# Kernel tuning notes

Hardware: AMD Instinct MI355X
Metric: run time of the kernel (lower is better)

Reference implementation:

```python
import jax, jax.numpy as jnp
import numpy as np

N_NODES = 100000
N_COMM = 1024
N_EDGES = 3200000
D_IN = 128
D_OUT = 128


def setup_inputs() -> dict:
    key = jax.random.key(0)
    k1, k2, k3, k4, k5, k6 = jax.random.split(key, 6)
    x = jax.random.normal(k1, (N_NODES + N_COMM, D_IN), dtype=jnp.float32)
    weight = jax.random.normal(k2, (D_IN, D_OUT), dtype=jnp.float32) * (1.0 / np.sqrt(D_IN))
    # assignments must be positive so row/col sums are nonzero
    assignments = jax.random.uniform(k3, (N_NODES, N_COMM), dtype=jnp.float32)
    edge_row = jax.random.randint(k4, (N_EDGES,), 0, N_NODES, dtype=jnp.int32)
    edge_col = jax.random.randint(k5, (N_EDGES,), 0, N_NODES, dtype=jnp.int32)
    edge_val = jax.random.uniform(k6, (N_EDGES,), dtype=jnp.float32)
    return {"x": x, "weight": weight, "assignments": assignments,
            "edge_row": edge_row, "edge_col": edge_col, "edge_val": edge_val}


def reference(x, weight, assignments, edge_row, edge_col, edge_val):
    N, C = assignments.shape
    support = x @ weight                      # [N+C, D_OUT]
    sup_nodes = support[:N]                   # node rows (support[:-C])
    sup_comm = support[N:]                    # community rows (support[-C:])

    # row-normalized assignments @ community support
    a_norm = assignments / assignments.sum(axis=1, keepdims=True)  # [N, C]
    comm_to_node = a_norm @ sup_comm                               # [N, D_OUT]

    # sparse adj @ node support via COO gather + segment scatter-add
    msgs = edge_val[:, None] * sup_nodes[edge_col]                 # [E, D_OUT]
    spmm = jax.ops.segment_sum(msgs, edge_row, num_segments=N)     # [N, D_OUT]

    output1 = comm_to_node + spmm                                  # [N, D_OUT]

    # row-normalized assignments.T @ node support
    at = assignments.T                                             # [C, N]
    at_norm = at / at.sum(axis=1, keepdims=True)
    output2 = at_norm @ sup_nodes                                  # [C, D_OUT]

    return jnp.concatenate((output1, output2), axis=0)            # [N+C, D_OUT]
```

## Files before the change

kernel.cpp:

```cpp
#include <hip/hip_runtime.h>
#include <hip/hip_fp16.h>

#define NN 100000
#define NC 1024
#define NM 101024
#define NE 3200000
#define DD 128

typedef __attribute__((ext_vector_type(8))) short s16x8;
typedef __attribute__((ext_vector_type(4))) float f32x4;

#define MFMA __builtin_amdgcn_mfma_f32_16x16x32_bf16

__device__ __forceinline__ short f2bf(float f) {
  unsigned u = __float_as_uint(f);
  u = (u + 0x7FFFu + ((u >> 16) & 1u)) >> 16;
  return (short)u;
}
__device__ __forceinline__ float bf2f(short h) {
  return __uint_as_float(((unsigned)(unsigned short)h) << 16);
}

__global__ __launch_bounds__(256) void k_zero(int* __restrict__ p, int n) {
  int t = blockIdx.x * 256 + threadIdx.x;
  if (t < n) p[t] = 0;
}

__global__ __launch_bounds__(256) void k_wpack(const float* __restrict__ W,
                                               short* __restrict__ wh,
                                               short* __restrict__ wl) {
  int t = blockIdx.x * 256 + threadIdx.x;
  int k = t >> 7, d = t & 127;
  float v = W[t];
  short h = f2bf(v);
  short l = f2bf(v - bf2f(h));
  int idx = (((k >> 5) * 8 + (d >> 4)) * 64 + ((k >> 3) & 3) * 16 + (d & 15)) * 8 + (k & 7);
  wh[idx] = h;
  wl[idx] = l;
}

__global__ __launch_bounds__(256) void k_support(const float* __restrict__ x,
                                                 const short* __restrict__ wh,
                                                 const short* __restrict__ wl,
                                                 float* __restrict__ sup) {
  int wave = threadIdx.x >> 6, lane = threadIdx.x & 63;
  int r0 = blockIdx.x * 64 + wave * 16;
  int arow = r0 + (lane & 15);
  if (arow >= NM) arow = NM - 1;
  int kb = (lane >> 4) * 8;
  f32x4 acc[8];
  #pragma unroll
  for (int dt = 0; dt < 8; ++dt)
    #pragma unroll
    for (int q = 0; q < 4; ++q) acc[dt][q] = 0.f;

  #pragma unroll
  for (int ks = 0; ks < 4; ++ks) {
    const float* ap = x + (size_t)arow * DD + ks * 32 + kb;
    float4 v0 = *(const float4*)ap;
    float4 v1 = *(const float4*)(ap + 4);
    float vv[8] = {v0.x, v0.y, v0.z, v0.w, v1.x, v1.y, v1.z, v1.w};
    s16x8 xh, xl;
    #pragma unroll
    for (int j = 0; j < 8; ++j) {
      short h = f2bf(vv[j]);
      xh[j] = h;
      xl[j] = f2bf(vv[j] - bf2f(h));
    }
    const short* bph = wh + ks * 4096 + lane * 8;
    const short* bpl = wl + ks * 4096 + lane * 8;
    #pragma unroll
    for (int dt = 0; dt < 8; ++dt) {
      s16x8 bh = *(const s16x8*)(bph + dt * 512);
      s16x8 bl = *(const s16x8*)(bpl + dt * 512);
      acc[dt] = MFMA(xh, bh, acc[dt], 0, 0, 0);
      acc[dt] = MFMA(xl, bh, acc[dt], 0, 0, 0);
      acc[dt] = MFMA(xh, bl, acc[dt], 0, 0, 0);
    }
  }
  int rg = (lane >> 4) * 4, cc = lane & 15;
  #pragma unroll
  for (int dt = 0; dt < 8; ++dt)
    #pragma unroll
    for (int q = 0; q < 4; ++q) {
      int rr = r0 + rg + q;
      if (rr < NM) sup[(size_t)rr * DD + dt * 16 + cc] = acc[dt][q];
    }
}

__global__ __launch_bounds__(256) void k_suph(const float* __restrict__ sup,
                                              unsigned* __restrict__ suph) {
  int t = blockIdx.x * 256 + threadIdx.x;
  float2 f = *(const float2*)(sup + (size_t)t * 2);
  __half2 h = __floats2half2_rn(f.x, f.y);
  suph[t] = *(unsigned*)&h;
}

__global__ __launch_bounds__(256) void k_spack(const float* __restrict__ sup,
                                               short* __restrict__ bpk) {
  int t = blockIdx.x * 256 + threadIdx.x;
  int d = t & 127, ib = t >> 7;
  int rb = ib >> 2, g = ib & 3;
  s16x8 o;
  #pragma unroll
  for (int j = 0; j < 8; ++j) o[j] = f2bf(sup[(size_t)(ib * 8 + j) * DD + d]);
  *(s16x8*)(bpk + (size_t)((rb * 8 + (d >> 4)) * 64 + g * 16 + (d & 15)) * 8) = o;
}

__global__ __launch_bounds__(256) void k_u1(const float* __restrict__ A,
                                            const short* __restrict__ bpk,
                                            float* __restrict__ out) {
  __shared__ float rsh[128];
  int wave = threadIdx.x >> 6, lane = threadIdx.x & 63;
  int r0 = blockIdx.x * 128 + wave * 32;
  int kb = (lane >> 4) * 8;
  f32x4 acc[2][8];
  #pragma unroll
  for (int m = 0; m < 2; ++m)
    #pragma unroll
    for (int dt = 0; dt < 8; ++dt)
      #pragma unroll
      for (int q = 0; q < 4; ++q) acc[m][dt][q] = 0.f;
  float rs[2] = {0.f, 0.f};
  int row[2];
  #pragma unroll
  for (int m = 0; m < 2; ++m) {
    int r = r0 + m * 16 + (lane & 15);
    row[m] = (r < NN) ? r : NN - 1;
  }
  for (int ks = 0; ks < 32; ++ks) {
    s16x8 af[2];
    #pragma unroll
    for (int m = 0; m < 2; ++m) {
      const float* ap = A + (size_t)row[m] * NC + ks * 32 + kb;
      float4 v0 = *(const float4*)ap;
      float4 v1 = *(const float4*)(ap + 4);
      rs[m] += v0.x + v0.y + v0.z + v0.w + v1.x + v1.y + v1.z + v1.w;
      af[m][0] = f2bf(v0.x); af[m][1] = f2bf(v0.y);
      af[m][2] = f2bf(v0.z); af[m][3] = f2bf(v0.w);
      af[m][4] = f2bf(v1.x); af[m][5] = f2bf(v1.y);
      af[m][6] = f2bf(v1.z); af[m][7] = f2bf(v1.w);
    }
    const short* bp = bpk + (size_t)(3125 + ks) * 4096 + lane * 8;
    #pragma unroll
    for (int dt = 0; dt < 8; ++dt) {
      s16x8 b = *(const s16x8*)(bp + dt * 512);
      acc[0][dt] = MFMA(af[0], b, acc[0][dt], 0, 0, 0);
      acc[1][dt] = MFMA(af[1], b, acc[1][dt], 0, 0, 0);
    }
  }
  #pragma unroll
  for (int m = 0; m < 2; ++m) {
    float v = rs[m];
    v += __shfl_xor(v, 16);
    v += __shfl_xor(v, 32);
    if (lane < 16) rsh[wave * 32 + m * 16 + lane] = v;
  }
  __syncthreads();
  int rg = (lane >> 4) * 4, cc = lane & 15;
  #pragma unroll
  for (int m = 0; m < 2; ++m)
    #pragma unroll
    for (int q = 0; q < 4; ++q) {
      int wr = wave * 32 + m * 16 + rg + q;
      int r = blockIdx.x * 128 + wr;
      if (r < NN) {
        float inv = 1.f / rsh[wr];
        #pragma unroll
        for (int dt = 0; dt < 8; ++dt)
          out[(size_t)r * DD + dt * 16 + cc] = acc[m][dt][q] * inv;
      }
    }
}

__global__ __launch_bounds__(256) void k_u2(const float* __restrict__ A,
                                            const short* __restrict__ bpk,
                                            float* __restrict__ u2,
                                            float* __restrict__ csum) {
  __shared__ short atile[2][128 * 40];
  int wave = threadIdx.x >> 6, lane = threadIdx.x & 63;
  int c0 = (blockIdx.x & 7) * 128;
  int s = blockIdx.x >> 3;
  int wc = wave * 32;
  f32x4 acc[2][8];
  #pragma unroll
  for (int m = 0; m < 2; ++m)
    #pragma unroll
    for (int dt = 0; dt < 8; ++dt)
      #pragma unroll
      for (int q = 0; q < 4; ++q) acc[m][dt][q] = 0.f;
  float cs[2] = {0.f, 0.f};
  int ld_i = threadIdx.x >> 5;
  int ld_c = (threadIdx.x & 31) * 4;

  float4 rv[4];
  #pragma unroll
  for (int it = 0; it < 4; ++it)
    rv[it] = *(const float4*)(A + (size_t)(s * 800 + it * 8 + ld_i) * NC + c0 + ld_c);
  #pragma unroll
  for (int it = 0; it < 4; ++it) {
    int i = it * 8 + ld_i;
    atile[0][(ld_c + 0) * 40 + i] = f2bf(rv[it].x);
    atile[0][(ld_c + 1) * 40 + i] = f2bf(rv[it].y);
    atile[0][(ld_c + 2) * 40 + i] = f2bf(rv[it].z);
    atile[0][(ld_c + 3) * 40 + i] = f2bf(rv[it].w);
  }
  __syncthreads();

  for (int kk = 0; kk < 25; ++kk) {
    int p = kk & 1;
    if (kk < 24) {
      int i0n = s * 800 + (kk + 1) * 32;
      #pragma unroll
      for (int it = 0; it < 4; ++it)
        rv[it] = *(const float4*)(A + (size_t)(i0n + it * 8 + ld_i) * NC + c0 + ld_c);
    }
    s16x8 af[2];
    #pragma unroll
    for (int m = 0; m < 2; ++m) {
      af[m] = *(const s16x8*)(&atile[p][(wc + m * 16 + (lane & 15)) * 40 + (lane >> 4) * 8]);
      #pragma unroll
      for (int j = 0; j < 8; ++j) cs[m] += bf2f(af[m][j]);
    }
    if (kk < 24) {
      #pragma unroll
      for (int it = 0; it < 4; ++it) {
        int i = it * 8 + ld_i;
        atile[p ^ 1][(ld_c + 0) * 40 + i] = f2bf(rv[it].x);
        atile[p ^ 1][(ld_c + 1) * 40 + i] = f2bf(rv[it].y);
        atile[p ^ 1][(ld_c + 2) * 40 + i] = f2bf(rv[it].z);
        atile[p ^ 1][(ld_c + 3) * 40 + i] = f2bf(rv[it].w);
      }
    }
    const short* bp = bpk + (size_t)(s * 25 + kk) * 4096 + lane * 8;
    #pragma unroll
    for (int dt = 0; dt < 8; ++dt) {
      s16x8 b = *(const s16x8*)(bp + dt * 512);
      acc[0][dt] = MFMA(af[0], b, acc[0][dt], 0, 0, 0);
      acc[1][dt] = MFMA(af[1], b, acc[1][dt], 0, 0, 0);
    }
    __syncthreads();
  }
  #pragma unroll
  for (int m = 0; m < 2; ++m) {
    float v = cs[m];
    v += __shfl_xor(v, 16);
    v += __shfl_xor(v, 32);
    if (lane < 16) atomicAdd(&csum[c0 + wc + m * 16 + lane], v);
  }
  int rg = (lane >> 4) * 4, cc = lane & 15;
  #pragma unroll
  for (int m = 0; m < 2; ++m)
    #pragma unroll
    for (int dt = 0; dt < 8; ++dt)
      #pragma unroll
      for (int q = 0; q < 4; ++q)
        atomicAdd(&u2[(size_t)(c0 + wc + m * 16 + rg + q) * DD + dt * 16 + cc],
                  acc[m][dt][q]);
}

__global__ __launch_bounds__(256) void k_out2(const float* __restrict__ u2,
                                              const float* __restrict__ csum,
                                              float* __restrict__ out) {
  int t = blockIdx.x * 256 + threadIdx.x;
  int c = t >> 7;
  out[(size_t)(NN + c) * DD + (t & 127)] = u2[t] / csum[c];
}

__global__ __launch_bounds__(256) void k_hist(const int* __restrict__ er, int* __restrict__ hist) {
  int t = blockIdx.x * 256 + threadIdx.x;
  if (t < NE) atomicAdd(&hist[er[t]], 1);
}

__global__ __launch_bounds__(256) void k_scan1(const int* __restrict__ hist,
                                               int* __restrict__ excl,
                                               int* __restrict__ bsum) {
  __shared__ int sm[256];
  int t = threadIdx.x, g = blockIdx.x * 256 + t;
  int v = (g < NN) ? hist[g] : 0;
  sm[t] = v;
  __syncthreads();
  for (int off = 1; off < 256; off <<= 1) {
    int u = (t >= off) ? sm[t - off] : 0;
    __syncthreads();
    sm[t] += u;
    __syncthreads();
  }
  if (g < NN) excl[g] = sm[t] - v;
  if (t == 255) bsum[blockIdx.x] = sm[255];
}

__global__ __launch_bounds__(512) void k_scan2(const int* __restrict__ bsum,
                                               int* __restrict__ boff, int nb) {
  __shared__ int sm[512];
  int t = threadIdx.x;
  int v = (t < nb) ? bsum[t] : 0;
  sm[t] = v;
  __syncthreads();
  for (int off = 1; off < 512; off <<= 1) {
    int u = (t >= off) ? sm[t - off] : 0;
    __syncthreads();
    sm[t] += u;
    __syncthreads();
  }
  if (t < nb) boff[t] = sm[t] - v;
}

__global__ __launch_bounds__(256) void k_scan3(const int* __restrict__ excl,
                                               const int* __restrict__ boff,
                                               int* __restrict__ offs,
                                               int* __restrict__ cur) {
  int t = threadIdx.x, g = blockIdx.x * 256 + t;
  if (g < NN) {
    int o = excl[g] + boff[blockIdx.x];
    offs[g] = o;
    cur[g] = o;
  }
  if (g == 0) offs[NN] = NE;
}

__global__ __launch_bounds__(256) void k_scatter(const int* __restrict__ er,
                                                 const int* __restrict__ ec,
                                                 const float* __restrict__ ev,
                                                 int* __restrict__ cur,
                                                 int2* __restrict__ pairs) {
  int t = blockIdx.x * 256 + threadIdx.x;
  if (t < NE) {
    int r = er[t];
    int p = atomicAdd(&cur[r], 1);
    pairs[p] = make_int2(ec[t], __float_as_int(ev[t]));
  }
}

__global__ __launch_bounds__(256) void k_spmm(const int* __restrict__ offs,
                                              const int2* __restrict__ pairs,
                                              const unsigned* __restrict__ suph,
                                              float* __restrict__ out) {
  int wave = threadIdx.x >> 6, lane = threadIdx.x & 63;
  int row = blockIdx.x * 4 + wave;
  int beg = offs[row], end = offs[row + 1];
  float ax = 0.f, ay = 0.f;
  int e = beg;
  for (; e + 4 <= end; e += 4) {
    int2 p0 = pairs[e], p1 = pairs[e + 1], p2 = pairs[e + 2], p3 = pairs[e + 3];
    unsigned g0 = suph[(size_t)p0.x * 64 + lane];
    unsigned g1 = suph[(size_t)p1.x * 64 + lane];
    unsigned g2 = suph[(size_t)p2.x * 64 + lane];
    unsigned g3 = suph[(size_t)p3.x * 64 + lane];
    float2 v0 = __half22float2(*(__half2*)&g0);
    float2 v1 = __half22float2(*(__half2*)&g1);
    float2 v2 = __half22float2(*(__half2*)&g2);
    float2 v3 = __half22float2(*(__half2*)&g3);
    float c0 = __int_as_float(p0.y), c1 = __int_as_float(p1.y);
    float c2 = __int_as_float(p2.y), c3 = __int_as_float(p3.y);
    ax = fmaf(c0, v0.x, ax); ay = fmaf(c0, v0.y, ay);
    ax = fmaf(c1, v1.x, ax); ay = fmaf(c1, v1.y, ay);
    ax = fmaf(c2, v2.x, ax); ay = fmaf(c2, v2.y, ay);
    ax = fmaf(c3, v3.x, ax); ay = fmaf(c3, v3.y, ay);
  }
  for (; e < end; ++e) {
    int2 p = pairs[e];
    unsigned g = suph[(size_t)p.x * 64 + lane];
    float2 v = __half22float2(*(__half2*)&g);
    float c = __int_as_float(p.y);
    ax = fmaf(c, v.x, ax);
    ay = fmaf(c, v.y, ay);
  }
  float2* o = (float2*)(out + (size_t)row * DD);
  float2 c = o[lane];
  c.x += ax;
  c.y += ay;
  o[lane] = c;
}

extern "C" void kernel_launch(void* const* d_in, const int* in_sizes, int n_in,
                              void* d_out, int out_size, void* d_ws, size_t ws_size,
                              hipStream_t stream) {
  const float* x  = (const float*)d_in[0];
  const float* W  = (const float*)d_in[1];
  const float* A  = (const float*)d_in[2];
  const int*   er = (const int*)d_in[3];
  const int*   ec = (const int*)d_in[4];
  const float* ev = (const float*)d_in[5];
  float* out = (float*)d_out;

  char* ws = (char*)d_ws;
  size_t off = 0;
  auto alloc = [&](size_t bytes) -> void* {
    off = (off + 255) & ~(size_t)255;
    void* p = ws + off;
    off += bytes;
    return p;
  };
  float*    sup   = (float*)alloc((size_t)NM * DD * 4);
  short*    bpk   = (short*)alloc((size_t)NM * DD * 2);
  unsigned* suphp = (unsigned*)alloc((size_t)NN * 64 * 4);
  short*    wh    = (short*)alloc(128 * 128 * 2);
  short*    wl    = (short*)alloc(128 * 128 * 2);
  float* u2    = (float*)alloc((size_t)NC * DD * 4);
  float* csum  = (float*)alloc(NC * 4);
  int*   hist  = (int*)alloc(NN * 4);
  int*   excl  = (int*)alloc(NN * 4);
  int*   offs  = (int*)alloc((NN + 1) * 4);
  int*   cur   = (int*)alloc(NN * 4);
  int*   bsum  = (int*)alloc(512 * 4);
  int*   boff  = (int*)alloc(512 * 4);
  int2*  pairs = (int2*)alloc((size_t)NE * 8);
  (void)ws_size; (void)in_sizes; (void)n_in; (void)out_size;

  const int ZN = NC * DD + NC + NN;
  k_zero<<<dim3((ZN + 255) / 256), dim3(256), 0, stream>>>((int*)u2, ZN);
  k_wpack<<<dim3(64), dim3(256), 0, stream>>>(W, wh, wl);
  k_support<<<dim3(1579), dim3(256), 0, stream>>>(x, wh, wl, sup);
  k_suph<<<dim3(25000), dim3(256), 0, stream>>>(sup, suphp);
  k_spack<<<dim3(6314), dim3(256), 0, stream>>>(sup, bpk);
  k_hist<<<dim3(12500), dim3(256), 0, stream>>>(er, hist);
  k_scan1<<<dim3(391), dim3(256), 0, stream>>>(hist, excl, bsum);
  k_scan2<<<dim3(1), dim3(512), 0, stream>>>(bsum, boff, 391);
  k_scan3<<<dim3(391), dim3(256), 0, stream>>>(excl, boff, offs, cur);
  k_scatter<<<dim3(12500), dim3(256), 0, stream>>>(er, ec, ev, cur, pairs);
  k_u1<<<dim3(782), dim3(256), 0, stream>>>(A, bpk, out);
  k_u2<<<dim3(1000), dim3(256), 0, stream>>>(A, bpk, u2, csum);
  k_out2<<<dim3(512), dim3(256), 0, stream>>>(u2, csum, out);
  k_spmm<<<dim3(25000), dim3(256), 0, stream>>>(offs, pairs, suphp, out);
}
```

Baseline: 1.380 ms.

## Replace CSR build and row SpMM with two-pass bucketed edge partition and LDS accumulation

Drops the histogram, three-pass scan and per-edge atomic scatter that built a full CSR. Edges are instead partitioned in two LDS-staged passes into 25 coarse and then 800 fine row buckets of 128 rows each, with fixed capacities per bucket. A new SpMM kernel gives each bucket and half of the feature columns to one block, which accumulates messages into a shared-memory tile with LDS atomics and then adds the tile into the output. The aim is to cut global atomics and scattered writes, at the cost of fixed bucket capacities (A1CAP, A2CAP) that overflow if edges are skewed, and LDS atomic contention.

```diff
diff --git a/kernel.cpp b/kernel.cpp
--- a/kernel.cpp
+++ b/kernel.cpp
@@ -7,6 +7,10 @@
 #define NE 3200000
 #define DD 128
 
+#define A1CAP 140000
+#define A2CAP 4608
+#define NB 782
+
 typedef __attribute__((ext_vector_type(8))) short s16x8;
 typedef __attribute__((ext_vector_type(4))) float f32x4;
 
@@ -24,6 +28,13 @@
 __global__ __launch_bounds__(256) void k_zero(int* __restrict__ p, int n) {
   int t = blockIdx.x * 256 + threadIdx.x;
   if (t < n) p[t] = 0;
+}
+
+__global__ __launch_bounds__(1024) void k_cinit(int* __restrict__ cur25,
+                                                int* __restrict__ cur800) {
+  int t = threadIdx.x;
+  if (t < 25) cur25[t] = t * A1CAP;
+  if (t < 800) cur800[t] = t * A2CAP;
 }
 
 __global__ __launch_bounds__(256) void k_wpack(const float* __restrict__ W,
@@ -267,110 +278,142 @@
   out[(size_t)(NN + c) * DD + (t & 127)] = u2[t] / csum[c];
 }
 
-__global__ __launch_bounds__(256) void k_hist(const int* __restrict__ er, int* __restrict__ hist) {
-  int t = blockIdx.x * 256 + threadIdx.x;
-  if (t < NE) atomicAdd(&hist[er[t]], 1);
-}
-
-__global__ __launch_bounds__(256) void k_scan1(const int* __restrict__ hist,
-                                               int* __restrict__ excl,
-                                               int* __restrict__ bsum) {
-  __shared__ int sm[256];
-  int t = threadIdx.x, g = blockIdx.x * 256 + t;
-  int v = (g < NN) ? hist[g] : 0;
-  sm[t] = v;
-  __syncthreads();
-  for (int off = 1; off < 256; off <<= 1) {
-    int u = (t >= off) ? sm[t - off] : 0;
+__global__ __launch_bounds__(256) void k_a1(const int* __restrict__ er,
+                                            const int* __restrict__ ec,
+                                            const float* __restrict__ ev,
+                                            int* __restrict__ cur25,
+                                            int2* __restrict__ a1buf) {
+  __shared__ int2 stg[25][320];
+  __shared__ int cnt[25];
+  int t = threadIdx.x, wave = t >> 6, lane = t & 63;
+  int beg = blockIdx.x * 6250, end = beg + 6250;
+  if (t < 25) cnt[t] = 0;
+  __syncthreads();
+  for (int b0 = beg; b0 < end; b0 += 256) {
+    int e = b0 + t;
+    if (e < end) {
+      int row = er[e];
+      int2 rec = make_int2(ec[e] | ((row & 4095) << 17), __float_as_int(ev[e]));
+      int s = row >> 12;
+      int slot = atomicAdd(&cnt[s], 1);
+      stg[s][slot] = rec;
+    }
     __syncthreads();
-    sm[t] += u;
+    for (int s = wave; s < 25; s += 4) {
+      int c = cnt[s];
+      if (c >= 64) {
+        int pos;
+        if (lane == 0) pos = atomicAdd(&cur25[s], c);
+        pos = __shfl(pos, 0);
+        for (int i = lane; i < c; i += 64) a1buf[pos + i] = stg[s][i];
+        if (lane == 0) cnt[s] = 0;
+      }
+    }
     __syncthreads();
   }
-  if (g < NN) excl[g] = sm[t] - v;
-  if (t == 255) bsum[blockIdx.x] = sm[255];
-}
-
-__global__ __launch_bounds__(512) void k_scan2(const int* __restrict__ bsum,
-                                               int* __restrict__ boff, int nb) {
-  __shared__ int sm[512];
-  int t = threadIdx.x;
-  int v = (t < nb) ? bsum[t] : 0;
-  sm[t] = v;
-  __syncthreads();
-  for (int off = 1; off < 512; off <<= 1) {
-    int u = (t >= off) ? sm[t - off] : 0;
+  for (int s = wave; s < 25; s += 4) {
+    int c = cnt[s];
+    if (c > 0) {
+      int pos;
+      if (lane == 0) pos = atomicAdd(&cur25[s], c);
+      pos = __shfl(pos, 0);
+      for (int i = lane; i < c; i += 64) a1buf[pos + i] = stg[s][i];
+    }
+  }
+}
+
+__global__ __launch_bounds__(128) void k_a2(const int2* __restrict__ a1buf,
+                                            const int* __restrict__ cur25,
+                                            int* __restrict__ cur800,
+                                            int2* __restrict__ a2buf) {
+  __shared__ int2 stg[32][255];
+  __shared__ int cnt[32];
+  int t = threadIdx.x, wave = t >> 6, lane = t & 63;
+  int s = blockIdx.x >> 6, j = blockIdx.x & 63;
+  int total = cur25[s] - s * A1CAP;
+  int chunk = (total + 63) >> 6;
+  int beg = j * chunk, end = min(total, beg + chunk);
+  const int2* rp = a1buf + (size_t)s * A1CAP;
+  if (t < 32) cnt[t] = 0;
+  __syncthreads();
+  for (int b0 = beg; b0 < end; b0 += 128) {
+    int e = b0 + t;
+    if (e < end) {
+      int2 rec = rp[e];
+      int sub = (rec.x >> 24) & 31;
+      int slot = atomicAdd(&cnt[sub], 1);
+      stg[sub][slot] = rec;
+    }
     __syncthreads();
-    sm[t] += u;
+    for (int sub = wave * 16; sub < wave * 16 + 16; ++sub) {
+      int c = cnt[sub];
+      if (c >= 128) {
+        int pos;
+        if (lane == 0) pos = atomicAdd(&cur800[(s << 5) + sub], c);
+        pos = __shfl(pos, 0);
+        for (int i = lane; i < c; i += 64) a2buf[pos + i] = stg[sub][i];
+        if (lane == 0) cnt[sub] = 0;
+      }
+    }
     __syncthreads();
   }
-  if (t < nb) boff[t] = sm[t] - v;
-}
-
-__global__ __launch_bounds__(256) void k_scan3(const int* __restrict__ excl,
-                                               const int* __restrict__ boff,
-                                               int* __restrict__ offs,
-                                               int* __restrict__ cur) {
-  int t = threadIdx.x, g = blockIdx.x * 256 + t;
-  if (g < NN) {
-    int o = excl[g] + boff[blockIdx.x];
-    offs[g] = o;
-    cur[g] = o;
-  }
-  if (g == 0) offs[NN] = NE;
-}
-
-__global__ __launch_bounds__(256) void k_scatter(const int* __restrict__ er,
-                                                 const int* __restrict__ ec,
-                                                 const float* __restrict__ ev,
-                                                 int* __restrict__ cur,
-                                                 int2* __restrict__ pairs) {
-  int t = blockIdx.x * 256 + threadIdx.x;
-  if (t < NE) {
-    int r = er[t];
-    int p = atomicAdd(&cur[r], 1);
-    pairs[p] = make_int2(ec[t], __float_as_int(ev[t]));
-  }
-}
-
-__global__ __launch_bounds__(256) void k_spmm(const int* __restrict__ offs,
-                                              const int2* __restrict__ pairs,
-                                              const unsigned* __restrict__ suph,
-                                              float* __restrict__ out) {
-  int wave = threadIdx.x >> 6, lane = threadIdx.x & 63;
-  int row = blockIdx.x * 4 + wave;
-  int beg = offs[row], end = offs[row + 1];
-  float ax = 0.f, ay = 0.f;
-  int e = beg;
-  for (; e + 4 <= end; e += 4) {
-    int2 p0 = pairs[e], p1 = pairs[e + 1], p2 = pairs[e + 2], p3 = pairs[e + 3];
-    unsigned g0 = suph[(size_t)p0.x * 64 + lane];
-    unsigned g1 = suph[(size_t)p1.x * 64 + lane];
-    unsigned g2 = suph[(size_t)p2.x * 64 + lane];
-    unsigned g3 = suph[(size_t)p3.x * 64 + lane];
-    float2 v0 = __half22float2(*(__half2*)&g0);
-    float2 v1 = __half22float2(*(__half2*)&g1);
-    float2 v2 = __half22float2(*(__half2*)&g2);
-    float2 v3 = __half22float2(*(__half2*)&g3);
-    float c0 = __int_as_float(p0.y), c1 = __int_as_float(p1.y);
-    float c2 = __int_as_float(p2.y), c3 = __int_as_float(p3.y);
-    ax = fmaf(c0, v0.x, ax); ay = fmaf(c0, v0.y, ay);
-    ax = fmaf(c1, v1.x, ax); ay = fmaf(c1, v1.y, ay);
-    ax = fmaf(c2, v2.x, ax); ay = fmaf(c2, v2.y, ay);
-    ax = fmaf(c3, v3.x, ax); ay = fmaf(c3, v3.y, ay);
-  }
-  for (; e < end; ++e) {
-    int2 p = pairs[e];
-    unsigned g = suph[(size_t)p.x * 64 + lane];
-    float2 v = __half22float2(*(__half2*)&g);
-    float c = __int_as_float(p.y);
-    ax = fmaf(c, v.x, ax);
-    ay = fmaf(c, v.y, ay);
-  }
-  float2* o = (float2*)(out + (size_t)row * DD);
-  float2 c = o[lane];
-  c.x += ax;
-  c.y += ay;
-  o[lane] = c;
+  for (int sub = wave * 16; sub < wave * 16 + 16; ++sub) {
+    int c = cnt[sub];
+    if (c > 0) {
+      int pos;
+      if (lane == 0) pos = atomicAdd(&cur800[(s << 5) + sub], c);
+      pos = __shfl(pos, 0);
+      for (int i = lane; i < c; i += 64) a2buf[pos + i] = stg[sub][i];
+    }
+  }
+}
+
+__global__ __launch_bounds__(256) void k_b(const int2* __restrict__ a2buf,
+                                           const int* __restrict__ cur800,
+                                           const unsigned short* __restrict__ suphh,
+                                           float* __restrict__ out) {
+  __shared__ float acc[128 * 64];
+  int t = threadIdx.x, wave = t >> 6, lane = t & 63;
+  int b = blockIdx.x >> 1, h = blockIdx.x & 1;
+  int cntb = cur800[b] - b * A2CAP;
+  const int2* rp = a2buf + (size_t)b * A2CAP;
+  #pragma unroll
+  for (int i = 0; i < 32; ++i) acc[i * 256 + t] = 0.f;
+  __syncthreads();
+
+  for (int b0 = wave * 64; b0 < cntb; b0 += 256) {
+    int idx = b0 + lane;
+    int2 rec = rp[min(idx, cntb - 1)];
+    if (idx >= cntb) rec.y = 0;
+    for (int j = 0; j < 64; j += 8) {
+      unsigned short g[8];
+      float vals[8];
+      int rls[8];
+      #pragma unroll
+      for (int u = 0; u < 8; ++u) {
+        int rx = __shfl(rec.x, j + u);
+        int ry = __shfl(rec.y, j + u);
+        vals[u] = __int_as_float(ry);
+        rls[u] = (rx >> 17) & 127;
+        g[u] = suphh[(size_t)(rx & 0x1FFFF) * 128 + (h << 6) + lane];
+      }
+      #pragma unroll
+      for (int u = 0; u < 8; ++u) {
+        __half hv = *reinterpret_cast<__half*>(&g[u]);
+        atomicAdd(&acc[rls[u] * 64 + lane], __half2float(hv) * vals[u]);
+      }
+    }
+  }
+  __syncthreads();
+  int col = t & 63, rg = t >> 6;
+  #pragma unroll 4
+  for (int rr = 0; rr < 32; ++rr) {
+    int row = b * 128 + rg * 32 + rr;
+    if (row < NN) {
+      size_t o = (size_t)row * 128 + (h << 6) + col;
+      out[o] += acc[(rg * 32 + rr) * 64 + col];
+    }
+  }
 }
 
 extern "C" void kernel_launch(void* const* d_in, const int* in_sizes, int n_in,
@@ -399,28 +442,23 @@
   short*    wl    = (short*)alloc(128 * 128 * 2);
   float* u2    = (float*)alloc((size_t)NC * DD * 4);
   float* csum  = (float*)alloc(NC * 4);
-  int*   hist  = (int*)alloc(NN * 4);
-  int*   excl  = (int*)alloc(NN * 4);
-  int*   offs  = (int*)alloc((NN + 1) * 4);
-  int*   cur   = (int*)alloc(NN * 4);
-  int*   bsum  = (int*)alloc(512 * 4);
-  int*   boff  = (int*)alloc(512 * 4);
-  int2*  pairs = (int2*)alloc((size_t)NE * 8);
+  int*   cur25 = (int*)alloc(25 * 4);
+  int*   cur800= (int*)alloc(800 * 4);
+  int2*  a1buf = (int2*)alloc((size_t)25 * A1CAP * 8);
+  int2*  a2buf = (int2*)alloc((size_t)800 * A2CAP * 8);
   (void)ws_size; (void)in_sizes; (void)n_in; (void)out_size;
 
-  const int ZN = NC * DD + NC + NN;
+  const int ZN = NC * DD + NC;
   k_zero<<<dim3((ZN + 255) / 256), dim3(256), 0, stream>>>((int*)u2, ZN);
+  k_cinit<<<dim3(1), dim3(1024), 0, stream>>>(cur25, cur800);
   k_wpack<<<dim3(64), dim3(256), 0, stream>>>(W, wh, wl);
   k_support<<<dim3(1579), dim3(256), 0, stream>>>(x, wh, wl, sup);
   k_suph<<<dim3(25000), dim3(256), 0, stream>>>(sup, suphp);
   k_spack<<<dim3(6314), dim3(256), 0, stream>>>(sup, bpk);
-  k_hist<<<dim3(12500), dim3(256), 0, stream>>>(er, hist);
-  k_scan1<<<dim3(391), dim3(256), 0, stream>>>(hist, excl, bsum);
-  k_scan2<<<dim3(1), dim3(512), 0, stream>>>(bsum, boff, 391);
-  k_scan3<<<dim3(391), dim3(256), 0, stream>>>(excl, boff, offs, cur);
-  k_scatter<<<dim3(12500), dim3(256), 0, stream>>>(er, ec, ev, cur, pairs);
+  k_a1<<<dim3(512), dim3(256), 0, stream>>>(er, ec, ev, cur25, a1buf);
+  k_a2<<<dim3(1600), dim3(128), 0, stream>>>(a1buf, cur25, cur800, a2buf);
   k_u1<<<dim3(782), dim3(256), 0, stream>>>(A, bpk, out);
   k_u2<<<dim3(1000), dim3(256), 0, stream>>>(A, bpk, u2, csum);
   k_out2<<<dim3(512), dim3(256), 0, stream>>>(u2, csum, out);
-  k_spmm<<<dim3(25000), dim3(256), 0, stream>>>(offs, pairs, suphp, out);
-}
+  k_b<<<dim3(NB * 2), dim3(256), 0, stream>>>(a2buf, cur800, (const unsigned short*)suphp, out);
+}
```

Measured after the change: 3.872 ms. 181% more time.

## Replace global-atomic COO-to-CSR scatter with two-pass bucketed radix scatter

Applied to the files above, without the earlier changes.

Edges are first partitioned into 25 coarse row buckets of 4096 rows. Each block stages records in LDS and flushes them in chunks to per-bucket regions using a global atomic per chunk, and the histogram is fused into the same pass. A second kernel then places each bucket's edges into CSR order using LDS atomic cursors, replacing 3.2M global atomics on scattered cursors. The second pass runs only 25 blocks, which limits parallelism, and it relies on a fixed per-bucket capacity and on packing the column into 17 bits.

```diff
diff --git a/kernel.cpp b/kernel.cpp
--- a/kernel.cpp
+++ b/kernel.cpp
@@ -7,6 +7,8 @@
 #define NE 3200000
 #define DD 128
 
+#define A1CAP 140000
+
 typedef __attribute__((ext_vector_type(8))) short s16x8;
 typedef __attribute__((ext_vector_type(4))) float f32x4;
 
@@ -24,6 +26,11 @@
 __global__ __launch_bounds__(256) void k_zero(int* __restrict__ p, int n) {
   int t = blockIdx.x * 256 + threadIdx.x;
   if (t < n) p[t] = 0;
+}
+
+__global__ __launch_bounds__(64) void k_cinit(int* __restrict__ cur25) {
+  int t = threadIdx.x;
+  if (t < 25) cur25[t] = t * A1CAP;
 }
 
 __global__ __launch_bounds__(256) void k_wpack(const float* __restrict__ W,
@@ -267,9 +274,50 @@
   out[(size_t)(NN + c) * DD + (t & 127)] = u2[t] / csum[c];
 }
 
-__global__ __launch_bounds__(256) void k_hist(const int* __restrict__ er, int* __restrict__ hist) {
-  int t = blockIdx.x * 256 + threadIdx.x;
-  if (t < NE) atomicAdd(&hist[er[t]], 1);
+__global__ __launch_bounds__(256) void k_a1(const int* __restrict__ er,
+                                            const int* __restrict__ ec,
+                                            const float* __restrict__ ev,
+                                            int* __restrict__ cur25,
+                                            int2* __restrict__ a1buf,
+                                            int* __restrict__ hist) {
+  __shared__ int2 stg[25][320];
+  __shared__ int cnt[25];
+  int t = threadIdx.x, wave = t >> 6, lane = t & 63;
+  int beg = blockIdx.x * 6250, end = beg + 6250;
+  if (t < 25) cnt[t] = 0;
+  __syncthreads();
+  for (int b0 = beg; b0 < end; b0 += 256) {
+    int e = b0 + t;
+    if (e < end) {
+      int row = er[e];
+      atomicAdd(&hist[row], 1);
+      int2 rec = make_int2(ec[e] | ((row & 4095) << 17), __float_as_int(ev[e]));
+      int s = row >> 12;
+      int slot = atomicAdd(&cnt[s], 1);
+      stg[s][slot] = rec;
+    }
+    __syncthreads();
+    for (int s = wave; s < 25; s += 4) {
+      int c = cnt[s];
+      if (c >= 64) {
+        int pos;
+        if (lane == 0) pos = atomicAdd(&cur25[s], c);
+        pos = __shfl(pos, 0);
+        for (int i = lane; i < c; i += 64) a1buf[pos + i] = stg[s][i];
+        if (lane == 0) cnt[s] = 0;
+      }
+    }
+    __syncthreads();
+  }
+  for (int s = wave; s < 25; s += 4) {
+    int c = cnt[s];
+    if (c > 0) {
+      int pos;
+      if (lane == 0) pos = atomicAdd(&cur25[s], c);
+      pos = __shfl(pos, 0);
+      for (int i = lane; i < c; i += 64) a1buf[pos + i] = stg[s][i];
+    }
+  }
 }
 
 __global__ __launch_bounds__(256) void k_scan1(const int* __restrict__ hist,
@@ -308,27 +356,33 @@
 
 __global__ __launch_bounds__(256) void k_scan3(const int* __restrict__ excl,
                                                const int* __restrict__ boff,
-                                               int* __restrict__ offs,
-                                               int* __restrict__ cur) {
+                                               int* __restrict__ offs) {
   int t = threadIdx.x, g = blockIdx.x * 256 + t;
-  if (g < NN) {
-    int o = excl[g] + boff[blockIdx.x];
-    offs[g] = o;
-    cur[g] = o;
-  }
+  if (g < NN) offs[g] = excl[g] + boff[blockIdx.x];
   if (g == 0) offs[NN] = NE;
 }
 
-__global__ __launch_bounds__(256) void k_scatter(const int* __restrict__ er,
-                                                 const int* __restrict__ ec,
-                                                 const float* __restrict__ ev,
-                                                 int* __restrict__ cur,
-                                                 int2* __restrict__ pairs) {
-  int t = blockIdx.x * 256 + threadIdx.x;
-  if (t < NE) {
-    int r = er[t];
-    int p = atomicAdd(&cur[r], 1);
-    pairs[p] = make_int2(ec[t], __float_as_int(ev[t]));
+__global__ __launch_bounds__(1024) void k_s2(const int2* __restrict__ a1buf,
+                                             const int* __restrict__ cur25,
+                                             const int* __restrict__ offs,
+                                             int2* __restrict__ pairs) {
+  __shared__ int cur[4096];
+  int t = threadIdx.x;
+  int s = blockIdx.x;
+  int rbase = s << 12;
+  #pragma unroll
+  for (int i = 0; i < 4; ++i) {
+    int r = rbase + i * 1024 + t;
+    cur[i * 1024 + t] = (r < NN) ? offs[r] : 0;
+  }
+  __syncthreads();
+  int total = cur25[s] - s * A1CAP;
+  const int2* rp = a1buf + (size_t)s * A1CAP;
+  for (int e = t; e < total; e += 1024) {
+    int2 rec = rp[e];
+    int rl = (rec.x >> 17) & 4095;
+    int pos = atomicAdd(&cur[rl], 1);
+    pairs[pos] = make_int2(rec.x & 0x1FFFF, rec.y);
   }
 }
 
@@ -402,23 +456,25 @@
   int*   hist  = (int*)alloc(NN * 4);
   int*   excl  = (int*)alloc(NN * 4);
   int*   offs  = (int*)alloc((NN + 1) * 4);
-  int*   cur   = (int*)alloc(NN * 4);
   int*   bsum  = (int*)alloc(512 * 4);
   int*   boff  = (int*)alloc(512 * 4);
+  int*   cur25 = (int*)alloc(25 * 4);
+  int2*  a1buf = (int2*)alloc((size_t)25 * A1CAP * 8);
   int2*  pairs = (int2*)alloc((size_t)NE * 8);
   (void)ws_size; (void)in_sizes; (void)n_in; (void)out_size;
 
   const int ZN = NC * DD + NC + NN;
   k_zero<<<dim3((ZN + 255) / 256), dim3(256), 0, stream>>>((int*)u2, ZN);
+  k_cinit<<<dim3(1), dim3(64), 0, stream>>>(cur25);
   k_wpack<<<dim3(64), dim3(256), 0, stream>>>(W, wh, wl);
   k_support<<<dim3(1579), dim3(256), 0, stream>>>(x, wh, wl, sup);
   k_suph<<<dim3(25000), dim3(256), 0, stream>>>(sup, suphp);
   k_spack<<<dim3(6314), dim3(256), 0, stream>>>(sup, bpk);
-  k_hist<<<dim3(12500), dim3(256), 0, stream>>>(er, hist);
+  k_a1<<<dim3(512), dim3(256), 0, stream>>>(er, ec, ev, cur25, a1buf, hist);
   k_scan1<<<dim3(391), dim3(256), 0, stream>>>(hist, excl, bsum);
   k_scan2<<<dim3(1), dim3(512), 0, stream>>>(bsum, boff, 391);
-  k_scan3<<<dim3(391), dim3(256), 0, stream>>>(excl, boff, offs, cur);
-  k_scatter<<<dim3(12500), dim3(256), 0, stream>>>(er, ec, ev, cur, pairs);
+  k_scan3<<<dim3(391), dim3(256), 0, stream>>>(excl, boff, offs);
+  k_s2<<<dim3(25), dim3(1024), 0, stream>>>(a1buf, cur25, offs, pairs);
   k_u1<<<dim3(782), dim3(256), 0, stream>>>(A, bpk, out);
   k_u2<<<dim3(1000), dim3(256), 0, stream>>>(A, bpk, u2, csum);
   k_out2<<<dim3(512), dim3(256), 0, stream>>>(u2, csum, out);
```

Measured after the change: 1.611 ms. 16.7% more time.

## Build CSR with a two-level bucket sort and reuse a bf16 copy of assignments

Applied to the files above, without the earlier changes.

Replaces the global-atomic histogram, three-pass scan and scatter with a two-level bucket sort. Edges are first binned into 49 row super-buckets per block in a buffer that aliases the support array. Per-bucket shared-memory histograms, scans and local scatters then produce the CSR offsets and pairs. Separately, k_u1 writes a bf16 copy of the assignment matrix so k_u2 reads half-width data instead of reconverting fp32. The bucket capacity of 120 silently drops edges if a block's bucket overflows. The second-stage kernels also run only 49 large blocks, which limits parallelism.

```diff
diff --git a/kernel.cpp b/kernel.cpp
--- a/kernel.cpp
+++ b/kernel.cpp
@@ -6,6 +6,10 @@
 #define NM 101024
 #define NE 3200000
 #define DD 128
+
+#define SB 49
+#define BCAP 120
+#define A1BLKS 1024
 
 typedef __attribute__((ext_vector_type(8))) short s16x8;
 typedef __attribute__((ext_vector_type(4))) float f32x4;
@@ -107,9 +111,101 @@
   *(s16x8*)(bpk + (size_t)((rb * 8 + (d >> 4)) * 64 + g * 16 + (d & 15)) * 8) = o;
 }
 
+__global__ __launch_bounds__(256) void k_a1(const int* __restrict__ er,
+                                            const int* __restrict__ ec,
+                                            const float* __restrict__ ev,
+                                            int* __restrict__ acnt,
+                                            int2* __restrict__ a1buf) {
+  __shared__ int cnt[SB];
+  int t = threadIdx.x;
+  if (t < SB) cnt[t] = 0;
+  __syncthreads();
+  int beg = blockIdx.x * 3125;
+  size_t bbase = (size_t)blockIdx.x * SB;
+  for (int e = beg + t; e < beg + 3125; e += 256) {
+    int row = er[e];
+    int2 rec = make_int2(ec[e] | ((row & 2047) << 17), __float_as_int(ev[e]));
+    int s = row >> 11;
+    int slot = atomicAdd(&cnt[s], 1);
+    if (slot < BCAP) a1buf[(bbase + s) * BCAP + slot] = rec;
+  }
+  __syncthreads();
+  if (t < SB) acnt[blockIdx.x * SB + t] = min(cnt[t], BCAP);
+}
+
+__global__ __launch_bounds__(1024) void k_hist2(const int2* __restrict__ a1buf,
+                                                const int* __restrict__ acnt,
+                                                int* __restrict__ lexcl,
+                                                int* __restrict__ tot) {
+  __shared__ int hist[2048];
+  __shared__ int ws2[1024];
+  int t = threadIdx.x, s = blockIdx.x;
+  hist[t] = 0; hist[t + 1024] = 0;
+  __syncthreads();
+  for (int i = t; i < A1BLKS * BCAP; i += 1024) {
+    int b = i / BCAP, j = i - b * BCAP;
+    if (j < acnt[b * SB + s]) {
+      int rx = a1buf[((size_t)b * SB + s) * BCAP + j].x;
+      atomicAdd(&hist[(rx >> 17) & 2047], 1);
+    }
+  }
+  __syncthreads();
+  int a = hist[2 * t], b2 = hist[2 * t + 1];
+  int v = a + b2;
+  ws2[t] = v;
+  __syncthreads();
+  for (int off = 1; off < 1024; off <<= 1) {
+    int u = (t >= off) ? ws2[t - off] : 0;
+    __syncthreads();
+    ws2[t] += u;
+    __syncthreads();
+  }
+  int excl = ws2[t] - v;
+  lexcl[s * 2048 + 2 * t] = excl;
+  lexcl[s * 2048 + 2 * t + 1] = excl + a;
+  if (t == 1023) tot[s] = ws2[1023];
+}
+
+__global__ void k_scan49(const int* __restrict__ tot, int* __restrict__ sbase,
+                         int* __restrict__ offs) {
+  if (threadIdx.x == 0) {
+    int acc = 0;
+    for (int s = 0; s < SB; ++s) { sbase[s] = acc; acc += tot[s]; }
+    offs[NN] = NE;
+  }
+}
+
+__global__ __launch_bounds__(1024) void k_s2b(const int2* __restrict__ a1buf,
+                                              const int* __restrict__ acnt,
+                                              const int* __restrict__ lexcl,
+                                              const int* __restrict__ sbase,
+                                              int* __restrict__ offs,
+                                              int2* __restrict__ pairs) {
+  __shared__ int cur[2048];
+  int t = threadIdx.x, s = blockIdx.x;
+  int rbase = s << 11;
+  int base = sbase[s];
+  for (int l = t; l < 2048; l += 1024) {
+    int o = base + lexcl[s * 2048 + l];
+    cur[l] = o;
+    int r = rbase + l;
+    if (r < NN) offs[r] = o;
+  }
+  __syncthreads();
+  for (int i = t; i < A1BLKS * BCAP; i += 1024) {
+    int b = i / BCAP, j = i - b * BCAP;
+    if (j < acnt[b * SB + s]) {
+      int2 rec = a1buf[((size_t)b * SB + s) * BCAP + j];
+      int pos = atomicAdd(&cur[(rec.x >> 17) & 2047], 1);
+      pairs[pos] = make_int2(rec.x & 0x1FFFF, rec.y);
+    }
+  }
+}
+
 __global__ __launch_bounds__(256) void k_u1(const float* __restrict__ A,
                                             const short* __restrict__ bpk,
-                                            float* __restrict__ out) {
+                                            float* __restrict__ out,
+                                            short* __restrict__ abf) {
   __shared__ float rsh[128];
   int wave = threadIdx.x >> 6, lane = threadIdx.x & 63;
   int r0 = blockIdx.x * 128 + wave * 32;
@@ -140,6 +236,7 @@
       af[m][2] = f2bf(v0.z); af[m][3] = f2bf(v0.w);
       af[m][4] = f2bf(v1.x); af[m][5] = f2bf(v1.y);
       af[m][6] = f2bf(v1.z); af[m][7] = f2bf(v1.w);
+      *(s16x8*)(abf + (size_t)row[m] * NC + ks * 32 + kb) = af[m];
     }
     const short* bp = bpk + (size_t)(3125 + ks) * 4096 + lane * 8;
     #pragma unroll
@@ -173,7 +270,7 @@
     }
 }
 
-__global__ __launch_bounds__(256) void k_u2(const float* __restrict__ A,
+__global__ __launch_bounds__(256) void k_u2(const short* __restrict__ abf,
                                             const short* __restrict__ bpk,
                                             float* __restrict__ u2,
                                             float* __restrict__ csum) {
@@ -190,21 +287,18 @@
       #pragma unroll
       for (int q = 0; q < 4; ++q) acc[m][dt][q] = 0.f;
   float cs[2] = {0.f, 0.f};
-  int ld_i = threadIdx.x >> 5;
-  int ld_c = (threadIdx.x & 31) * 4;
-
-  float4 rv[4];
-  #pragma unroll
-  for (int it = 0; it < 4; ++it)
-    rv[it] = *(const float4*)(A + (size_t)(s * 800 + it * 8 + ld_i) * NC + c0 + ld_c);
-  #pragma unroll
-  for (int it = 0; it < 4; ++it) {
-    int i = it * 8 + ld_i;
-    atile[0][(ld_c + 0) * 40 + i] = f2bf(rv[it].x);
-    atile[0][(ld_c + 1) * 40 + i] = f2bf(rv[it].y);
-    atile[0][(ld_c + 2) * 40 + i] = f2bf(rv[it].z);
-    atile[0][(ld_c + 3) * 40 + i] = f2bf(rv[it].w);
-  }
+  int li = threadIdx.x >> 4;
+  int lc = (threadIdx.x & 15) * 8;
+
+  s16x8 rv[2];
+  #pragma unroll
+  for (int it = 0; it < 2; ++it)
+    rv[it] = *(const s16x8*)(abf + (size_t)(s * 800 + it * 16 + li) * NC + c0 + lc);
+  #pragma unroll
+  for (int it = 0; it < 2; ++it)
+    #pragma unroll
+    for (int j = 0; j < 8; ++j)
+      atile[0][(lc + j) * 40 + it * 16 + li] = rv[it][j];
   __syncthreads();
 
   for (int kk = 0; kk < 25; ++kk) {
@@ -212,8 +306,8 @@
     if (kk < 24) {
       int i0n = s * 800 + (kk + 1) * 32;
       #pragma unroll
-      for (int it = 0; it < 4; ++it)
-        rv[it] = *(const float4*)(A + (size_t)(i0n + it * 8 + ld_i) * NC + c0 + ld_c);
+      for (int it = 0; it < 2; ++it)
+        rv[it] = *(const s16x8*)(abf + (size_t)(i0n + it * 16 + li) * NC + c0 + lc);
     }
     s16x8 af[2];
     #pragma unroll
@@ -224,13 +318,10 @@
     }
     if (kk < 24) {
       #pragma unroll
-      for (int it = 0; it < 4; ++it) {
-        int i = it * 8 + ld_i;
-        atile[p ^ 1][(ld_c + 0) * 40 + i] = f2bf(rv[it].x);
-        atile[p ^ 1][(ld_c + 1) * 40 + i] = f2bf(rv[it].y);
-        atile[p ^ 1][(ld_c + 2) * 40 + i] = f2bf(rv[it].z);
-        atile[p ^ 1][(ld_c + 3) * 40 + i] = f2bf(rv[it].w);
-      }
+      for (int it = 0; it < 2; ++it)
+        #pragma unroll
+        for (int j = 0; j < 8; ++j)
+          atile[p ^ 1][(lc + j) * 40 + it * 16 + li] = rv[it][j];
     }
     const short* bp = bpk + (size_t)(s * 25 + kk) * 4096 + lane * 8;
     #pragma unroll
@@ -265,71 +356,6 @@
   int t = blockIdx.x * 256 + threadIdx.x;
   int c = t >> 7;
   out[(size_t)(NN + c) * DD + (t & 127)] = u2[t] / csum[c];
-}
-
-__global__ __launch_bounds__(256) void k_hist(const int* __restrict__ er, int* __restrict__ hist) {
-  int t = blockIdx.x * 256 + threadIdx.x;
-  if (t < NE) atomicAdd(&hist[er[t]], 1);
-}
-
-__global__ __launch_bounds__(256) void k_scan1(const int* __restrict__ hist,
-                                               int* __restrict__ excl,
-                                               int* __restrict__ bsum) {
-  __shared__ int sm[256];
-  int t = threadIdx.x, g = blockIdx.x * 256 + t;
-  int v = (g < NN) ? hist[g] : 0;
-  sm[t] = v;
-  __syncthreads();
-  for (int off = 1; off < 256; off <<= 1) {
-    int u = (t >= off) ? sm[t - off] : 0;
-    __syncthreads();
-    sm[t] += u;
-    __syncthreads();
-  }
-  if (g < NN) excl[g] = sm[t] - v;
-  if (t == 255) bsum[blockIdx.x] = sm[255];
-}
-
-__global__ __launch_bounds__(512) void k_scan2(const int* __restrict__ bsum,
-                                               int* __restrict__ boff, int nb) {
-  __shared__ int sm[512];
-  int t = threadIdx.x;
-  int v = (t < nb) ? bsum[t] : 0;
-  sm[t] = v;
-  __syncthreads();
-  for (int off = 1; off < 512; off <<= 1) {
-    int u = (t >= off) ? sm[t - off] : 0;
-    __syncthreads();
-    sm[t] += u;
-    __syncthreads();
-  }
-  if (t < nb) boff[t] = sm[t] - v;
-}
-
-__global__ __launch_bounds__(256) void k_scan3(const int* __restrict__ excl,
-                                               const int* __restrict__ boff,
-                                               int* __restrict__ offs,
-                                               int* __restrict__ cur) {
-  int t = threadIdx.x, g = blockIdx.x * 256 + t;
-  if (g < NN) {
-    int o = excl[g] + boff[blockIdx.x];
-    offs[g] = o;
-    cur[g] = o;
-  }
-  if (g == 0) offs[NN] = NE;
-}
-
-__global__ __launch_bounds__(256) void k_scatter(const int* __restrict__ er,
-                                                 const int* __restrict__ ec,
-                                                 const float* __restrict__ ev,
-                                                 int* __restrict__ cur,
-                                                 int2* __restrict__ pairs) {
-  int t = blockIdx.x * 256 + threadIdx.x;
-  if (t < NE) {
-    int r = er[t];
-    int p = atomicAdd(&cur[r], 1);
-    pairs[p] = make_int2(ec[t], __float_as_int(ev[t]));
-  }
 }
 
 __global__ __launch_bounds__(256) void k_spmm(const int* __restrict__ offs,
@@ -399,28 +425,28 @@
   short*    wl    = (short*)alloc(128 * 128 * 2);
   float* u2    = (float*)alloc((size_t)NC * DD * 4);
   float* csum  = (float*)alloc(NC * 4);
-  int*   hist  = (int*)alloc(NN * 4);
-  int*   excl  = (int*)alloc(NN * 4);
+  short* abf   = (short*)alloc((size_t)NN * NC * 2);
+  int*   acnt  = (int*)alloc((size_t)A1BLKS * SB * 4);
+  int*   lexcl = (int*)alloc((size_t)SB * 2048 * 4);
+  int*   tot   = (int*)alloc(SB * 4);
+  int*   sbase = (int*)alloc(SB * 4);
   int*   offs  = (int*)alloc((NN + 1) * 4);
-  int*   cur   = (int*)alloc(NN * 4);
-  int*   bsum  = (int*)alloc(512 * 4);
-  int*   boff  = (int*)alloc(512 * 4);
   int2*  pairs = (int2*)alloc((size_t)NE * 8);
+  int2*  a1buf = (int2*)sup;
   (void)ws_size; (void)in_sizes; (void)n_in; (void)out_size;
 
-  const int ZN = NC * DD + NC + NN;
+  const int ZN = NC * DD + NC;
   k_zero<<<dim3((ZN + 255) / 256), dim3(256), 0, stream>>>((int*)u2, ZN);
   k_wpack<<<dim3(64), dim3(256), 0, stream>>>(W, wh, wl);
   k_support<<<dim3(1579), dim3(256), 0, stream>>>(x, wh, wl, sup);
   k_suph<<<dim3(25000), dim3(256), 0, stream>>>(sup, suphp);
   k_spack<<<dim3(6314), dim3(256), 0, stream>>>(sup, bpk);
-  k_hist<<<dim3(12500), dim3(256), 0, stream>>>(er, hist);
-  k_scan1<<<dim3(391), dim3(256), 0, stream>>>(hist, excl, bsum);
-  k_scan2<<<dim3(1), dim3(512), 0, stream>>>(bsum, boff, 391);
-  k_scan3<<<dim3(391), dim3(256), 0, stream>>>(excl, boff, offs, cur);
-  k_scatter<<<dim3(12500), dim3(256), 0, stream>>>(er, ec, ev, cur, pairs);
-  k_u1<<<dim3(782), dim3(256), 0, stream>>>(A, bpk, out);
-  k_u2<<<dim3(1000), dim3(256), 0, stream>>>(A, bpk, u2, csum);
+  k_a1<<<dim3(A1BLKS), dim3(256), 0, stream>>>(er, ec, ev, acnt, a1buf);
+  k_hist2<<<dim3(SB), dim3(1024), 0, stream>>>(a1buf, acnt, lexcl, tot);
+  k_scan49<<<dim3(1), dim3(64), 0, stream>>>(tot, sbase, offs);
+  k_s2b<<<dim3(SB), dim3(1024), 0, stream>>>(a1buf, acnt, lexcl, sbase, offs, pairs);
+  k_u1<<<dim3(782), dim3(256), 0, stream>>>(A, bpk, out, abf);
+  k_u2<<<dim3(1000), dim3(256), 0, stream>>>(abf, bpk, u2, csum);
   k_out2<<<dim3(512), dim3(256), 0, stream>>>(u2, csum, out);
   k_spmm<<<dim3(25000), dim3(256), 0, stream>>>(offs, pairs, suphp, out);
 }
```

Result: no change. 1.388 ms (+0.6%).
